# Kernel tuning notes

Measured on AMD Instinct MI355X. Metric: run time of the kernel, lower is better.

## Reference

```python
import jax, jax.numpy as jnp
import numpy as np

NU, NI = 100000, 50000          # sampled users / items in the block
E = 1600000                      # edges (user-item interactions)
D = 64                           # hidden_dims
R = 6                            # num_ratings + 1


def setup_inputs() -> dict:
    key = jax.random.key(0)
    ks = jax.random.split(key, 24)
    f = jax.random.normal
    inp = {
        'user_ids': jax.random.randint(ks[0], (NU,), 0, 500000),
        'item_ids': jax.random.randint(ks[1], (NI,), 0, 200000),
        'gender': jax.random.randint(ks[2], (NU,), 0, 3),
        'genres': jax.random.randint(ks[3], (NI,), 0, 20),
        'edge_user': jax.random.randint(ks[4], (E,), 0, NU),
        'edge_item': jax.random.randint(ks[5], (E,), 0, NI),
        'rating': jax.random.randint(ks[6], (E,), 0, R),
        'user_emb': f(ks[7], (500000, D), jnp.float32),
        'item_emb': f(ks[8], (200000, D), jnp.float32),
        'gender_emb': f(ks[9], (3, D), jnp.float32),
        'genre_emb': f(ks[10], (20, D), jnp.float32),
        'Wr_watched': f(ks[11], (R, D, D), jnp.float32) * 0.1,
        'Wr_watchedby': f(ks[12], (R, D, D), jnp.float32) * 0.1,
        'Ww': f(ks[13], (D, 2 * D), jnp.float32) * 0.1,
        'bw': f(ks[14], (D,), jnp.float32) * 0.1,
        'Wwb': f(ks[15], (D, 2 * D), jnp.float32) * 0.1,
        'bwb': f(ks[16], (D,), jnp.float32) * 0.1,
        'Wf': f(ks[17], (D, D), jnp.float32) * 0.1,
        'bf': f(ks[18], (D,), jnp.float32) * 0.1,
        'Vf': f(ks[19], (D, D), jnp.float32) * 0.1,
        'bv': f(ks[20], (D,), jnp.float32) * 0.1,
    }
    return inp


def _gcmc_conv(Wr, Wlin, blin, h_src, h_dst, src_idx, dst_idx, rating, n_dst):
    # per-node relation transform: [R, N_src, D] (grouped GEMM instead of per-edge [E,D,D])
    X = jnp.einsum('nj,rij->rni', h_src, Wr)
    m = X[rating, src_idx]                              # per-edge message [E, D]
    s = jax.ops.segment_sum(m, dst_idx, num_segments=n_dst)
    cnt = jax.ops.segment_sum(jnp.ones((m.shape[0], 1), m.dtype), dst_idx,
                              num_segments=n_dst)
    h_neigh = s / jnp.maximum(cnt, 1.0)                 # mean; 0 for isolated nodes
    return jax.nn.relu(jnp.concatenate([h_dst, h_neigh], axis=1) @ Wlin.T + blin)


def reference(user_ids, item_ids, gender, genres, edge_user, edge_item, rating,
              user_emb, item_emb, gender_emb, genre_emb,
              Wr_watched, Wr_watchedby, Ww, bw, Wwb, bwb, Wf, bf, Vf, bv):
    hu = user_emb[user_ids] + gender_emb[gender]        # [NU, D]
    hi = item_emb[item_ids] + genre_emb[genres]         # [NI, D]
    # GCMCLayer: 'watched' (user -> item) and 'watchedby' (item -> user)
    hi_new = _gcmc_conv(Wr_watched, Ww, bw, hu, hi, edge_user, edge_item,
                        rating, hi.shape[0])
    hu_new = _gcmc_conv(Wr_watchedby, Wwb, bwb, hi, hu, edge_item, edge_user,
                        rating, hu.shape[0])
    user_out = hu_new @ Wf.T + bf
    item_out = hi_new @ Vf.T + bv
    return user_out, item_out
```

## Files before the change

### kernel.cpp

```cpp
#include <hip/hip_runtime.h>
#include <hip/hip_bf16.h>

#define D 64
#define NRAT 6

typedef float f32x4 __attribute__((ext_vector_type(4)));
typedef short bf16x8 __attribute__((ext_vector_type(8)));

union FragU { uint32_t u[4]; bf16x8 v; };

__device__ __forceinline__ short f2bf(float f) {
    __hip_bfloat16 h = __float2bfloat16(f);
    union { __hip_bfloat16 h; short s; } c; c.h = h; return c.s;
}
__device__ __forceinline__ uint32_t pk2(float a, float b) {
    union { short s[2]; uint32_t u; } c; c.s[0] = f2bf(a); c.s[1] = f2bf(b); return c.u;
}

__global__ void build_setup(const int* __restrict__ uid, const int* __restrict__ iid,
                            const int* __restrict__ gender, const int* __restrict__ genres,
                            const float* __restrict__ user_emb, const float* __restrict__ item_emb,
                            const float* __restrict__ gender_emb, const float* __restrict__ genre_emb,
                            unsigned short* __restrict__ hu, unsigned short* __restrict__ hi,
                            int* __restrict__ zeroRegion,
                            const float* __restrict__ Wr_w, const float* __restrict__ Wr_wb,
                            const float* __restrict__ Ww, const float* __restrict__ Wwb,
                            const float* __restrict__ Vf, const float* __restrict__ Wf,
                            short* __restrict__ pWrW, short* __restrict__ pWrWB,
                            short* __restrict__ pWw, short* __restrict__ pWwb,
                            short* __restrict__ pVf, short* __restrict__ pWf,
                            int NU, int NI) {
    int t = blockIdx.x * blockDim.x + threadIdx.x;
    if (t < 512) zeroRegion[t] = 0;

    int tp = t - 1024;
    if (tp >= 0 && tp < 73728) {
        const float* src; short* dst; int K; int idx;
        if      (tp < 24576) { src = Wr_w;  dst = pWrW;  K = 64;  idx = tp; }
        else if (tp < 49152) { src = Wr_wb; dst = pWrWB; K = 64;  idx = tp - 24576; }
        else if (tp < 57344) { src = Ww;    dst = pWw;   K = 128; idx = tp - 49152; }
        else if (tp < 65536) { src = Wwb;   dst = pWwb;  K = 128; idx = tp - 57344; }
        else if (tp < 69632) { src = Vf;    dst = pVf;   K = 64;  idx = tp - 65536; }
        else                 { src = Wf;    dst = pWf;   K = 64;  idx = tp - 69632; }
        int per  = 64 * K;
        int sub  = idx / per;
        int li   = idx % per;
        int e    = li & 7;
        int lane = (li >> 3) & 63;
        int frag = li >> 9;
        int nkt  = K >> 5;
        int t16  = frag / nkt, tk = frag % nkt;
        int row  = t16 * 16 + (lane & 15);
        int col  = tk * 32 + (lane >> 4) * 8 + e;
        dst[idx] = f2bf(src[((size_t)(sub * 64 + row)) * K + col]);
    }

    int total = (NU + NI) * 16;
    if (t >= total) return;
    int row = t >> 4, c = t & 15;
    uint2 o;
    if (row < NU) {
        int u = uid[row], g = gender[row];
        float4 a = ((const float4*)user_emb)[(size_t)u * 16 + c];
        float4 b = ((const float4*)gender_emb)[(size_t)g * 16 + c];
        o.x = pk2(a.x + b.x, a.y + b.y); o.y = pk2(a.z + b.z, a.w + b.w);
        ((uint2*)hu)[(size_t)row * 16 + c] = o;
    } else {
        int r2 = row - NU;
        int it = iid[r2], ge = genres[r2];
        float4 a = ((const float4*)item_emb)[(size_t)it * 16 + c];
        float4 b = ((const float4*)genre_emb)[(size_t)ge * 16 + c];
        o.x = pk2(a.x + b.x, a.y + b.y); o.y = pk2(a.z + b.z, a.w + b.w);
        ((uint2*)hi)[(size_t)r2 * 16 + c] = o;
    }
}

__global__ __launch_bounds__(256) void hist_both(const int* __restrict__ edge_item,
                                                 const int* __restrict__ edge_user,
                                                 int* __restrict__ cntI, int* __restrict__ cntU,
                                                 int E) {
    __shared__ int hI[256], hU[256];
    hI[threadIdx.x] = 0; hU[threadIdx.x] = 0;
    __syncthreads();
    for (int i = blockIdx.x * blockDim.x + threadIdx.x; i < E; i += gridDim.x * blockDim.x) {
        atomicAdd(&hI[edge_item[i] >> 8], 1);
        atomicAdd(&hU[edge_user[i] >> 9], 1);
    }
    __syncthreads();
    int vi = hI[threadIdx.x], vu = hU[threadIdx.x];
    if (vi) atomicAdd(&cntI[threadIdx.x], vi);
    if (vu) atomicAdd(&cntU[threadIdx.x], vu);
}

__global__ __launch_bounds__(256) void scan_both(const int* __restrict__ cntI,
                                                 const int* __restrict__ cntU,
                                                 int* __restrict__ offI, int* __restrict__ offU,
                                                 int* __restrict__ curI, int* __restrict__ curU,
                                                 int NBI, int NBU, int E) {
    const int* cnt = blockIdx.x ? cntU : cntI;
    int* coarseOff  = blockIdx.x ? offU : offI;
    int* coarseCur  = blockIdx.x ? curU : curI;
    int NB          = blockIdx.x ? NBU : NBI;
    __shared__ int p[256];
    int tid = threadIdx.x;
    int v = (tid < NB) ? cnt[tid] : 0;
    p[tid] = v; __syncthreads();
    for (int dd = 1; dd < 256; dd <<= 1) {
        int a = (tid >= dd) ? p[tid - dd] : 0;
        __syncthreads();
        p[tid] += a;
        __syncthreads();
    }
    int excl = p[tid] - v;
    if (tid < NB) { coarseOff[tid] = excl; coarseCur[tid] = excl; }
    if (tid == 0) coarseOff[NB] = E;
}

__global__ __launch_bounds__(256) void multisplit_A2(
        const int* __restrict__ edge_item, const int* __restrict__ edge_user,
        const int* __restrict__ rating,
        int* __restrict__ curI, int* __restrict__ curU,
        unsigned* __restrict__ staged1, unsigned* __restrict__ staged2,
        int E, int nTiles, int NU, int NI) {
    const bool dirU = blockIdx.x >= nTiles;
    const int* dst = dirU ? edge_user : edge_item;
    const int* src = dirU ? edge_item : edge_user;
    const int shift = dirU ? 9 : 8;
    const int Ns = dirU ? NI : NU;
    int* coarseCur = dirU ? curU : curI;
    unsigned* staged = dirU ? staged2 : staged1;
    const int tile = (dirU ? blockIdx.x - nTiles : blockIdx.x) * 2048;

    __shared__ unsigned srt[2048];
    __shared__ int sft[2048];
    __shared__ int hist[256], pfx[256], shm[256];
    const int tid = threadIdx.x;
    int cnt = E - tile; if (cnt > 2048) cnt = 2048;
    hist[tid] = 0;
    __syncthreads();
    unsigned rec[8]; int bk[8];
    #pragma unroll
    for (int k = 0; k < 8; ++k) {
        int i = tile + k * 256 + tid;
        bk[k] = -1;
        if (i < E) {
            int d = dst[i], s = src[i], r = rating[i];
            bk[k] = d >> shift;
            rec[k] = (unsigned)(s + r * Ns) | ((unsigned)(d & ((1 << shift) - 1)) << 20);
            atomicAdd(&hist[bk[k]], 1);
        }
    }
    __syncthreads();
    pfx[tid] = hist[tid];
    __syncthreads();
    for (int dd = 1; dd < 256; dd <<= 1) {
        int a = (tid >= dd) ? pfx[tid - dd] : 0;
        __syncthreads();
        pfx[tid] += a;
        __syncthreads();
    }
    int h = hist[tid];
    int excl = pfx[tid] - h;
    int gb = 0;
    if (h > 0) gb = atomicAdd(&coarseCur[tid], h);
    shm[tid] = gb - excl;
    __syncthreads();
    hist[tid] = excl;
    __syncthreads();
    #pragma unroll
    for (int k = 0; k < 8; ++k) {
        if (bk[k] >= 0) {
            int p = atomicAdd(&hist[bk[k]], 1);
            srt[p] = rec[k];
            sft[p] = shm[bk[k]];
        }
    }
    __syncthreads();
    for (int i = tid; i < cnt; i += 256)
        staged[sft[i] + i] = srt[i];
}

__global__ __launch_bounds__(256) void multisplit_B2(
        unsigned* __restrict__ staged1, unsigned* __restrict__ staged2,
        const int* __restrict__ coarseOffI, const int* __restrict__ coarseOffU,
        int* __restrict__ offI, int* __restrict__ offU,
        int NBI, int NU, int NI, int E) {
    const bool dirU = (int)blockIdx.x >= NBI;
    unsigned* staged = dirU ? staged2 : staged1;
    const int* coarseOff = dirU ? coarseOffU : coarseOffI;
    int* off = dirU ? offU : offI;
    const int N = dirU ? NU : NI;
    const int shift = dirU ? 9 : 8;
    const int b = dirU ? blockIdx.x - NBI : blockIdx.x;
    const int nb = dirU ? (N + (1 << 9) - 1) >> 9 : NBI;

    __shared__ unsigned rec[16384];
    __shared__ int hist[512], pfx[512];
    const int tid = threadIdx.x;
    const int range = 1 << shift;
    int cbase = coarseOff[b];
    int cnt = coarseOff[b + 1] - cbase;
    if (cnt > 16384) cnt = 16384;
    hist[tid] = 0; hist[tid + 256] = 0;
    __syncthreads();
    for (int i = tid; i < cnt; i += 256) {
        unsigned x = staged[cbase + i];
        rec[i] = x;
        atomicAdd(&hist[x >> 20], 1);
    }
    __syncthreads();
    pfx[tid] = hist[tid]; pfx[tid + 256] = hist[tid + 256];
    __syncthreads();
    for (int dd = 1; dd < 256; dd <<= 1) {
        int a = (tid >= dd) ? pfx[tid - dd] : 0;
        int c = (tid >= dd) ? pfx[tid + 256 - dd] : 0;
        __syncthreads();
        pfx[tid] += a; pfx[tid + 256] += c;
        __syncthreads();
    }
    int tot0 = pfx[255];
    __syncthreads();
    pfx[tid + 256] += tot0;
    __syncthreads();
    int e0 = pfx[tid] - hist[tid];
    int e1 = pfx[tid + 256] - hist[tid + 256];
    __syncthreads();
    hist[tid] = e0; hist[tid + 256] = e1;
    int dbase = b << shift;
    if (dbase + tid < N) off[dbase + tid] = cbase + e0;
    if (range > 256 && dbase + tid + 256 < N) off[dbase + tid + 256] = cbase + e1;
    if (b == nb - 1 && tid == 0) off[N] = E;
    __syncthreads();
    for (int i = tid; i < cnt; i += 256) {
        unsigned x = rec[i];
        int p = atomicAdd(&hist[x >> 20], 1);
        staged[cbase + p] = x;
    }
}

__global__ __launch_bounds__(256) void pretransform2(
        const unsigned short* __restrict__ hu, const unsigned short* __restrict__ hi,
        const short* __restrict__ pWrW, const short* __restrict__ pWrWB,
        unsigned short* __restrict__ y1, unsigned short* __restrict__ y2,
        int NU, int NI, int wavesU) {
    const int lane = threadIdx.x & 63;
    const int m = lane & 15, q = lane >> 4;
    int wave = (blockIdx.x * blockDim.x + threadIdx.x) >> 6;
    const bool dirI = wave >= wavesU;
    const unsigned short* h = dirI ? hi : hu;
    const short* pWr = dirI ? pWrWB : pWrW;
    unsigned short* y = dirI ? y2 : y1;
    const int Ns = dirI ? NI : NU;
    if (dirI) wave -= wavesU;
    const int n0 = wave * 16;
    if (n0 >= Ns) return;
    int nrow = n0 + m; if (nrow > Ns - 1) nrow = Ns - 1;

    bf16x8 bB[2];
    {
        const unsigned short* ph = h + (size_t)nrow * D + q * 8;
        bB[0] = *(const bf16x8*)(ph);
        bB[1] = *(const bf16x8*)(ph + 32);
    }
    const int srcA = ((q & 1) << 5) + m;
    const int srcB = srcA + 16;
    const bool hiq = (q >> 1) != 0;

    #pragma unroll
    for (int r = 0; r < NRAT; ++r) {
        f32x4 acc[4] = {};
        #pragma unroll
        for (int it = 0; it < 4; ++it)
            #pragma unroll
            for (int kt = 0; kt < 2; ++kt) {
                bf16x8 a = *(const bf16x8*)(pWr + (((r * 4 + it) * 2 + kt) << 9) + (lane << 3));
                acc[it] = __builtin_amdgcn_mfma_f32_16x16x32_bf16(a, bB[kt], acc[it], 0, 0, 0);
            }
        uint32_t u0[4], u1[4];
        #pragma unroll
        for (int it = 0; it < 4; ++it) {
            u0[it] = pk2(acc[it][0], acc[it][1]);
            u1[it] = pk2(acc[it][2], acc[it][3]);
        }
        #pragma unroll
        for (int w = 0; w < 2; ++w) {
            uint32_t aa0 = (uint32_t)__shfl((int)u0[2*w],   srcA), bb0 = (uint32_t)__shfl((int)u0[2*w+1], srcA);
            uint32_t aa1 = (uint32_t)__shfl((int)u1[2*w],   srcA), bb1 = (uint32_t)__shfl((int)u1[2*w+1], srcA);
            uint32_t aa2 = (uint32_t)__shfl((int)u0[2*w],   srcB), bb2 = (uint32_t)__shfl((int)u0[2*w+1], srcB);
            uint32_t aa3 = (uint32_t)__shfl((int)u1[2*w],   srcB), bb3 = (uint32_t)__shfl((int)u1[2*w+1], srcB);
            FragU f;
            f.u[0] = hiq ? bb0 : aa0;
            f.u[1] = hiq ? bb1 : aa1;
            f.u[2] = hiq ? bb2 : aa2;
            f.u[3] = hiq ? bb3 : aa3;
            *(bf16x8*)(y + ((size_t)r * Ns + nrow) * D + w * 32 + q * 8) = f.v;
        }
    }
}

__global__ __launch_bounds__(256) void gather_both(
        const int* __restrict__ offI, const int* __restrict__ offU,
        const unsigned* __restrict__ staged1, const unsigned* __restrict__ staged2,
        const unsigned* __restrict__ y1, const unsigned* __restrict__ y2,
        unsigned* __restrict__ hn1, unsigned* __restrict__ hn2,
        int NI, int NU) {
    const int lane = threadIdx.x & 63;
    const int half = lane >> 5;
    const int l5   = lane & 31;
    int g = (blockIdx.x * blockDim.x + threadIdx.x) >> 6;
    const bool dirU = g >= NI;
    int n = dirU ? g - NI : g;
    if (dirU && n >= NU) return;
    const int* off = dirU ? offU : offI;
    const unsigned* packed = dirU ? staged2 : staged1;
    const unsigned* y = dirU ? y2 : y1;
    unsigned* hn = dirU ? hn2 : hn1;

    int b = off[n], e = off[n + 1];
    float a0 = 0.f, a1 = 0.f;

#define YPAIR(mm) y[(((mm) << 5) & 0x1FFFFE0u) | (unsigned)l5]
#define ACC2(dd) { a0 += __uint_as_float((dd) << 16); \
                   a1 += __uint_as_float((dd) & 0xFFFF0000u); }

    for (int base = b; base < e; base += 64) {
        int idx = base + lane; if (idx > e - 1) idx = e - 1;
        unsigned meta = packed[idx];
        int cnt = e - base; if (cnt > 64) cnt = 64;
        int j = 0;
        for (; j + 4 <= cnt; j += 4) {
            unsigned mA = (unsigned)__shfl((int)meta, j + half);
            unsigned mB = (unsigned)__shfl((int)meta, j + 2 + half);
            unsigned dA = YPAIR(mA);
            unsigned dB = YPAIR(mB);
            ACC2(dA); ACC2(dB);
        }
        if (j + 2 <= cnt) {
            unsigned mA = (unsigned)__shfl((int)meta, j + half);
            unsigned dA = YPAIR(mA);
            ACC2(dA);
            j += 2;
        }
        if (j < cnt) {
            unsigned mm = (unsigned)__builtin_amdgcn_readlane((int)meta, j);
            if (half == 0) { unsigned dd = YPAIR(mm); ACC2(dd); }
        }
    }
#undef YPAIR
#undef ACC2

    float o0 = __shfl(a0, lane ^ 32);
    float o1 = __shfl(a1, lane ^ 32);
    float inv = 1.0f / fmaxf((float)(e - b), 1.0f);
    float s0 = (a0 + o0) * inv;
    float s1 = (a1 + o1) * inv;
    if (lane < 32) hn[(size_t)n * 32 + l5] = pk2(s0, s1);
}

__global__ __launch_bounds__(256) void transform_both(
        const unsigned short* __restrict__ hn1, const unsigned short* __restrict__ hn2,
        const unsigned short* __restrict__ hi, const unsigned short* __restrict__ hu,
        const short* __restrict__ pWw, const short* __restrict__ pWwb,
        const float* __restrict__ bw, const float* __restrict__ bwb,
        const short* __restrict__ pVf, const short* __restrict__ pWf,
        const float* __restrict__ bv, const float* __restrict__ bf,
        float* __restrict__ item_out, float* __restrict__ user_out,
        int NI, int NU, int tilesI) {
    const int lane = threadIdx.x & 63;
    const int m = lane & 15, q = lane >> 4;
    int wave = (blockIdx.x * blockDim.x + threadIdx.x) >> 6;
    const bool dirU = wave >= tilesI;
    if (dirU) wave -= tilesI;
    const unsigned short* hn = dirU ? hn2 : hn1;
    const unsigned short* hd = dirU ? hu : hi;
    const short* pWlin = dirU ? pWwb : pWw;
    const float* blin  = dirU ? bwb : bw;
    const short* pW2   = dirU ? pWf : pVf;
    const float* b2    = dirU ? bf : bv;
    float* out = dirU ? user_out : item_out;
    const int N = dirU ? NU : NI;
    const int n0 = wave * 16;
    if (n0 >= N) return;
    int nrow = n0 + m; if (nrow > N - 1) nrow = N - 1;

    bf16x8 bH[2], bHN[2];
    {
        const unsigned short* ph = hd + (size_t)nrow * D + q * 8;
        bH[0] = *(const bf16x8*)(ph);
        bH[1] = *(const bf16x8*)(ph + 32);
        const unsigned short* pn = hn + (size_t)nrow * D + q * 8;
        bHN[0] = *(const bf16x8*)(pn);
        bHN[1] = *(const bf16x8*)(pn + 32);
    }

    f32x4 acc2[4] = {};
    #pragma unroll
    for (int it = 0; it < 4; ++it)
        #pragma unroll
        for (int kt = 0; kt < 4; ++kt) {
            bf16x8 a = *(const bf16x8*)(pWlin + (((it * 4) + kt) << 9) + (lane << 3));
            bf16x8 b = (kt < 2) ? bH[kt] : bHN[kt - 2];
            acc2[it] = __builtin_amdgcn_mfma_f32_16x16x32_bf16(a, b, acc2[it], 0, 0, 0);
        }

    const int srcA = ((q & 1) << 5) + m;
    const int srcB = srcA + 16;
    const bool hiq = (q >> 1) != 0;
    uint32_t u0[4], u1[4];
    float vbl = blin[lane];
    #pragma unroll
    for (int it = 0; it < 4; ++it) {
        float h0 = fmaxf(acc2[it][0] + __shfl(vbl, it * 16 + q * 4 + 0), 0.f);
        float h1 = fmaxf(acc2[it][1] + __shfl(vbl, it * 16 + q * 4 + 1), 0.f);
        float h2 = fmaxf(acc2[it][2] + __shfl(vbl, it * 16 + q * 4 + 2), 0.f);
        float h3 = fmaxf(acc2[it][3] + __shfl(vbl, it * 16 + q * 4 + 3), 0.f);
        u0[it] = pk2(h0, h1);
        u1[it] = pk2(h2, h3);
    }
    bf16x8 bA3[2];
    #pragma unroll
    for (int w = 0; w < 2; ++w) {
        uint32_t aa0 = (uint32_t)__shfl((int)u0[2*w],   srcA), bb0 = (uint32_t)__shfl((int)u0[2*w+1], srcA);
        uint32_t aa1 = (uint32_t)__shfl((int)u1[2*w],   srcA), bb1 = (uint32_t)__shfl((int)u1[2*w+1], srcA);
        uint32_t aa2 = (uint32_t)__shfl((int)u0[2*w],   srcB), bb2 = (uint32_t)__shfl((int)u0[2*w+1], srcB);
        uint32_t aa3 = (uint32_t)__shfl((int)u1[2*w],   srcB), bb3 = (uint32_t)__shfl((int)u1[2*w+1], srcB);
        FragU f;
        f.u[0] = hiq ? bb0 : aa0;
        f.u[1] = hiq ? bb1 : aa1;
        f.u[2] = hiq ? bb2 : aa2;
        f.u[3] = hiq ? bb3 : aa3;
        bA3[w] = f.v;
    }

    f32x4 acc3[4] = {};
    #pragma unroll
    for (int ct = 0; ct < 4; ++ct)
        #pragma unroll
        for (int kt = 0; kt < 2; ++kt) {
            bf16x8 b = *(const bf16x8*)(pW2 + (((ct * 2) + kt) << 9) + (lane << 3));
            acc3[ct] = __builtin_amdgcn_mfma_f32_16x16x32_bf16(bA3[kt], b, acc3[ct], 0, 0, 0);
        }
    #pragma unroll
    for (int ct = 0; ct < 4; ++ct) {
        float bb = b2[ct * 16 + m];
        #pragma unroll
        for (int rg = 0; rg < 4; ++rg) {
            int n = n0 + q * 4 + rg;
            if (n < N) out[(size_t)n * D + ct * 16 + m] = acc3[ct][rg] + bb;
        }
    }
}

extern "C" void kernel_launch(void* const* d_in, const int* in_sizes, int n_in,
                              void* d_out, int out_size, void* d_ws, size_t ws_size,
                              hipStream_t stream) {
    const int*   user_ids   = (const int*)  d_in[0];
    const int*   item_ids   = (const int*)  d_in[1];
    const int*   gender     = (const int*)  d_in[2];
    const int*   genres     = (const int*)  d_in[3];
    const int*   edge_user  = (const int*)  d_in[4];
    const int*   edge_item  = (const int*)  d_in[5];
    const int*   rating     = (const int*)  d_in[6];
    const float* user_emb   = (const float*)d_in[7];
    const float* item_emb   = (const float*)d_in[8];
    const float* gender_emb = (const float*)d_in[9];
    const float* genre_emb  = (const float*)d_in[10];
    const float* Wr_watched   = (const float*)d_in[11];
    const float* Wr_watchedby = (const float*)d_in[12];
    const float* Ww  = (const float*)d_in[13];
    const float* bw  = (const float*)d_in[14];
    const float* Wwb = (const float*)d_in[15];
    const float* bwb = (const float*)d_in[16];
    const float* Wf  = (const float*)d_in[17];
    const float* bf  = (const float*)d_in[18];
    const float* Vf  = (const float*)d_in[19];
    const float* bv  = (const float*)d_in[20];

    const int NU = in_sizes[0];
    const int NI = in_sizes[1];
    const int E  = in_sizes[4];
    const int NBI = (NI + 255) >> 8;
    const int NBU = (NU + 511) >> 9;

    float* out_f    = (float*)d_out;
    float* user_out = out_f;
    float* item_out = out_f + (size_t)NU * D;

    unsigned short* hu  = (unsigned short*)d_ws;
    unsigned short* hi  = hu  + (size_t)NU * D;
    unsigned short* hn1 = hi  + (size_t)NI * D;
    unsigned short* hn2 = hn1 + (size_t)NI * D;
    unsigned short* y1  = hn2 + (size_t)NU * D;
    unsigned short* y2  = y1  + (size_t)NRAT * NU * D;
    size_t bfElems = (size_t)(2 * NU + 2 * NI) * D + (size_t)NRAT * (NU + NI) * D;
    size_t byteOff = (bfElems * 2 + 15) & ~(size_t)15;
    short* pWrW  = (short*)((char*)d_ws + byteOff);
    short* pWrWB = pWrW  + 24576;
    short* pWw   = pWrWB + 24576;
    short* pWwb  = pWw   + 8192;
    short* pVf   = pWwb  + 8192;
    short* pWf   = pVf   + 4096;
    int* coarseCntI = (int*)(pWf + 4096);
    int* coarseCntU = coarseCntI + 256;
    int* coarseOffI = coarseCntU + 256;
    int* coarseOffU = coarseOffI + 257;
    int* coarseCurI = coarseOffU + 257;
    int* coarseCurU = coarseCurI + 256;
    int* offI   = coarseCurU + 256;
    int* offU   = offI + NI + 1;
    unsigned* staged1 = (unsigned*)(offU + NU + 1);
    unsigned* staged2 = staged1 + E;

    int totalh = (NU + NI) * 16;
    build_setup<<<(totalh + 255) / 256, 256, 0, stream>>>(
        user_ids, item_ids, gender, genres,
        user_emb, item_emb, gender_emb, genre_emb, hu, hi, coarseCntI,
        Wr_watched, Wr_watchedby, Ww, Wwb, Vf, Wf,
        pWrW, pWrWB, pWw, pWwb, pVf, pWf, NU, NI);

    hist_both<<<512, 256, 0, stream>>>(edge_item, edge_user, coarseCntI, coarseCntU, E);
    scan_both<<<2, 256, 0, stream>>>(coarseCntI, coarseCntU, coarseOffI, coarseOffU,
                                     coarseCurI, coarseCurU, NBI, NBU, E);

    const int nTilesA = (E + 2047) / 2048;
    multisplit_A2<<<2 * nTilesA, 256, 0, stream>>>(edge_item, edge_user, rating,
                                                   coarseCurI, coarseCurU,
                                                   staged1, staged2, E, nTilesA, NU, NI);
    multisplit_B2<<<NBI + NBU, 256, 0, stream>>>(staged1, staged2, coarseOffI, coarseOffU,
                                                 offI, offU, NBI, NU, NI, E);

    {
        int wavesU = (NU + 15) / 16, wavesI = (NI + 15) / 16;
        int blocks = (wavesU + wavesI + 3) / 4;
        pretransform2<<<blocks, 256, 0, stream>>>(hu, hi, pWrW, pWrWB, y1, y2, NU, NI, wavesU);
    }
    gather_both<<<(NI + NU + 3) / 4, 256, 0, stream>>>(offI, offU, staged1, staged2,
                                                       (const unsigned*)y1, (const unsigned*)y2,
                                                       (unsigned*)hn1, (unsigned*)hn2, NI, NU);
    {
        int tilesI = (NI + 15) / 16, tilesU = (NU + 15) / 16;
        int blocks = (tilesI + tilesU + 3) / 4;
        transform_both<<<blocks, 256, 0, stream>>>(hn1, hn2, hi, hu, pWw, pWwb, bw, bwb,
                                                   pVf, pWf, bv, bf, item_out, user_out,
                                                   NI, NU, tilesI);
    }
}
```

Before: 236.6 us.

## Fuse pretransform into multisplit launch and widen gather to four edges per step

The per-rating pretransform GEMM moves into the multisplit_A launch as extra blocks. This removes one kernel launch and lets the MFMA work overlap the bucketing pass. The gather kernel now has each quarter-wave load 8 bytes per lane (uint2), so four edges are processed per step instead of two. The partial sums are then reduced with xor shuffles. The fused kernel carries the multisplit's shared-memory footprint on the transform blocks, which may reduce their occupancy.

```diff
diff --git a/kernel.cpp b/kernel.cpp
--- a/kernel.cpp
+++ b/kernel.cpp
@@ -116,25 +116,86 @@
     if (tid == 0) coarseOff[NB] = E;
 }
 
-__global__ __launch_bounds__(256) void multisplit_A2(
+__global__ __launch_bounds__(256) void msA_pre(
         const int* __restrict__ edge_item, const int* __restrict__ edge_user,
         const int* __restrict__ rating,
         int* __restrict__ curI, int* __restrict__ curU,
         unsigned* __restrict__ staged1, unsigned* __restrict__ staged2,
-        int E, int nTiles, int NU, int NI) {
-    const bool dirU = blockIdx.x >= nTiles;
+        const unsigned short* __restrict__ hu, const unsigned short* __restrict__ hi,
+        const short* __restrict__ pWrW, const short* __restrict__ pWrWB,
+        unsigned short* __restrict__ y1, unsigned short* __restrict__ y2,
+        int E, int nTiles, int NU, int NI, int wavesU) {
+    __shared__ unsigned srt[2048];
+    __shared__ int sft[2048];
+    __shared__ int hist[256], pfx[256], shm[256];
+    const int tid = threadIdx.x;
+
+    if ((int)blockIdx.x >= 2 * nTiles) {
+        const int lane = tid & 63;
+        const int m = lane & 15, q = lane >> 4;
+        int wave = (((int)blockIdx.x - 2 * nTiles) * 256 + tid) >> 6;
+        const bool dirI = wave >= wavesU;
+        const unsigned short* h = dirI ? hi : hu;
+        const short* pWr = dirI ? pWrWB : pWrW;
+        unsigned short* y = dirI ? y2 : y1;
+        const int Ns = dirI ? NI : NU;
+        if (dirI) wave -= wavesU;
+        const int n0 = wave * 16;
+        if (n0 >= Ns) return;
+        int nrow = n0 + m; if (nrow > Ns - 1) nrow = Ns - 1;
+
+        bf16x8 bB[2];
+        {
+            const unsigned short* ph = h + (size_t)nrow * D + q * 8;
+            bB[0] = *(const bf16x8*)(ph);
+            bB[1] = *(const bf16x8*)(ph + 32);
+        }
+        const int srcA = ((q & 1) << 5) + m;
+        const int srcB = srcA + 16;
+        const bool hiq = (q >> 1) != 0;
+
+        #pragma unroll
+        for (int r = 0; r < NRAT; ++r) {
+            f32x4 acc[4] = {};
+            #pragma unroll
+            for (int it = 0; it < 4; ++it)
+                #pragma unroll
+                for (int kt = 0; kt < 2; ++kt) {
+                    bf16x8 a = *(const bf16x8*)(pWr + (((r * 4 + it) * 2 + kt) << 9) + (lane << 3));
+                    acc[it] = __builtin_amdgcn_mfma_f32_16x16x32_bf16(a, bB[kt], acc[it], 0, 0, 0);
+                }
+            uint32_t u0[4], u1[4];
+            #pragma unroll
+            for (int it = 0; it < 4; ++it) {
+                u0[it] = pk2(acc[it][0], acc[it][1]);
+                u1[it] = pk2(acc[it][2], acc[it][3]);
+            }
+            #pragma unroll
+            for (int w = 0; w < 2; ++w) {
+                uint32_t aa0 = (uint32_t)__shfl((int)u0[2*w],   srcA), bb0 = (uint32_t)__shfl((int)u0[2*w+1], srcA);
+                uint32_t aa1 = (uint32_t)__shfl((int)u1[2*w],   srcA), bb1 = (uint32_t)__shfl((int)u1[2*w+1], srcA);
+                uint32_t aa2 = (uint32_t)__shfl((int)u0[2*w],   srcB), bb2 = (uint32_t)__shfl((int)u0[2*w+1], srcB);
+                uint32_t aa3 = (uint32_t)__shfl((int)u1[2*w],   srcB), bb3 = (uint32_t)__shfl((int)u1[2*w+1], srcB);
+                FragU f;
+                f.u[0] = hiq ? bb0 : aa0;
+                f.u[1] = hiq ? bb1 : aa1;
+                f.u[2] = hiq ? bb2 : aa2;
+                f.u[3] = hiq ? bb3 : aa3;
+                *(bf16x8*)(y + ((size_t)r * Ns + nrow) * D + w * 32 + q * 8) = f.v;
+            }
+        }
+        return;
+    }
+
+    const bool dirU = (int)blockIdx.x >= nTiles;
     const int* dst = dirU ? edge_user : edge_item;
     const int* src = dirU ? edge_item : edge_user;
     const int shift = dirU ? 9 : 8;
     const int Ns = dirU ? NI : NU;
     int* coarseCur = dirU ? curU : curI;
     unsigned* staged = dirU ? staged2 : staged1;
-    const int tile = (dirU ? blockIdx.x - nTiles : blockIdx.x) * 2048;
-
-    __shared__ unsigned srt[2048];
-    __shared__ int sft[2048];
-    __shared__ int hist[256], pfx[256], shm[256];
-    const int tid = threadIdx.x;
+    const int tile = (dirU ? (int)blockIdx.x - nTiles : (int)blockIdx.x) * 2048;
+
     int cnt = E - tile; if (cnt > 2048) cnt = 2048;
     hist[tid] = 0;
     __syncthreads();
@@ -238,90 +299,32 @@
     }
 }
 
-__global__ __launch_bounds__(256) void pretransform2(
-        const unsigned short* __restrict__ hu, const unsigned short* __restrict__ hi,
-        const short* __restrict__ pWrW, const short* __restrict__ pWrWB,
-        unsigned short* __restrict__ y1, unsigned short* __restrict__ y2,
-        int NU, int NI, int wavesU) {
-    const int lane = threadIdx.x & 63;
-    const int m = lane & 15, q = lane >> 4;
-    int wave = (blockIdx.x * blockDim.x + threadIdx.x) >> 6;
-    const bool dirI = wave >= wavesU;
-    const unsigned short* h = dirI ? hi : hu;
-    const short* pWr = dirI ? pWrWB : pWrW;
-    unsigned short* y = dirI ? y2 : y1;
-    const int Ns = dirI ? NI : NU;
-    if (dirI) wave -= wavesU;
-    const int n0 = wave * 16;
-    if (n0 >= Ns) return;
-    int nrow = n0 + m; if (nrow > Ns - 1) nrow = Ns - 1;
-
-    bf16x8 bB[2];
-    {
-        const unsigned short* ph = h + (size_t)nrow * D + q * 8;
-        bB[0] = *(const bf16x8*)(ph);
-        bB[1] = *(const bf16x8*)(ph + 32);
-    }
-    const int srcA = ((q & 1) << 5) + m;
-    const int srcB = srcA + 16;
-    const bool hiq = (q >> 1) != 0;
-
-    #pragma unroll
-    for (int r = 0; r < NRAT; ++r) {
-        f32x4 acc[4] = {};
-        #pragma unroll
-        for (int it = 0; it < 4; ++it)
-            #pragma unroll
-            for (int kt = 0; kt < 2; ++kt) {
-                bf16x8 a = *(const bf16x8*)(pWr + (((r * 4 + it) * 2 + kt) << 9) + (lane << 3));
-                acc[it] = __builtin_amdgcn_mfma_f32_16x16x32_bf16(a, bB[kt], acc[it], 0, 0, 0);
-            }
-        uint32_t u0[4], u1[4];
-        #pragma unroll
-        for (int it = 0; it < 4; ++it) {
-            u0[it] = pk2(acc[it][0], acc[it][1]);
-            u1[it] = pk2(acc[it][2], acc[it][3]);
-        }
-        #pragma unroll
-        for (int w = 0; w < 2; ++w) {
-            uint32_t aa0 = (uint32_t)__shfl((int)u0[2*w],   srcA), bb0 = (uint32_t)__shfl((int)u0[2*w+1], srcA);
-            uint32_t aa1 = (uint32_t)__shfl((int)u1[2*w],   srcA), bb1 = (uint32_t)__shfl((int)u1[2*w+1], srcA);
-            uint32_t aa2 = (uint32_t)__shfl((int)u0[2*w],   srcB), bb2 = (uint32_t)__shfl((int)u0[2*w+1], srcB);
-            uint32_t aa3 = (uint32_t)__shfl((int)u1[2*w],   srcB), bb3 = (uint32_t)__shfl((int)u1[2*w+1], srcB);
-            FragU f;
-            f.u[0] = hiq ? bb0 : aa0;
-            f.u[1] = hiq ? bb1 : aa1;
-            f.u[2] = hiq ? bb2 : aa2;
-            f.u[3] = hiq ? bb3 : aa3;
-            *(bf16x8*)(y + ((size_t)r * Ns + nrow) * D + w * 32 + q * 8) = f.v;
-        }
-    }
-}
-
 __global__ __launch_bounds__(256) void gather_both(
         const int* __restrict__ offI, const int* __restrict__ offU,
         const unsigned* __restrict__ staged1, const unsigned* __restrict__ staged2,
-        const unsigned* __restrict__ y1, const unsigned* __restrict__ y2,
-        unsigned* __restrict__ hn1, unsigned* __restrict__ hn2,
+        const uint2* __restrict__ y1, const uint2* __restrict__ y2,
+        uint2* __restrict__ hn1, uint2* __restrict__ hn2,
         int NI, int NU) {
     const int lane = threadIdx.x & 63;
-    const int half = lane >> 5;
-    const int l5   = lane & 31;
+    const int qt = lane >> 4;
+    const int t  = lane & 15;
     int g = (blockIdx.x * blockDim.x + threadIdx.x) >> 6;
     const bool dirU = g >= NI;
     int n = dirU ? g - NI : g;
     if (dirU && n >= NU) return;
     const int* off = dirU ? offU : offI;
     const unsigned* packed = dirU ? staged2 : staged1;
-    const unsigned* y = dirU ? y2 : y1;
-    unsigned* hn = dirU ? hn2 : hn1;
+    const uint2* y = dirU ? y2 : y1;
+    uint2* hn = dirU ? hn2 : hn1;
 
     int b = off[n], e = off[n + 1];
-    float a0 = 0.f, a1 = 0.f;
-
-#define YPAIR(mm) y[(((mm) << 5) & 0x1FFFFE0u) | (unsigned)l5]
-#define ACC2(dd) { a0 += __uint_as_float((dd) << 16); \
-                   a1 += __uint_as_float((dd) & 0xFFFF0000u); }
+    float a0 = 0.f, a1 = 0.f, a2 = 0.f, a3 = 0.f;
+
+#define YROW(mm) y[(((mm) & 0xFFFFFu) << 4) | (unsigned)t]
+#define ACC4(dd) { a0 += __uint_as_float((dd).x << 16);          \
+                   a1 += __uint_as_float((dd).x & 0xFFFF0000u);  \
+                   a2 += __uint_as_float((dd).y << 16);          \
+                   a3 += __uint_as_float((dd).y & 0xFFFF0000u); }
 
     for (int base = b; base < e; base += 64) {
         int idx = base + lane; if (idx > e - 1) idx = e - 1;
@@ -329,32 +332,32 @@
         int cnt = e - base; if (cnt > 64) cnt = 64;
         int j = 0;
         for (; j + 4 <= cnt; j += 4) {
-            unsigned mA = (unsigned)__shfl((int)meta, j + half);
-            unsigned mB = (unsigned)__shfl((int)meta, j + 2 + half);
-            unsigned dA = YPAIR(mA);
-            unsigned dB = YPAIR(mB);
-            ACC2(dA); ACC2(dB);
-        }
-        if (j + 2 <= cnt) {
-            unsigned mA = (unsigned)__shfl((int)meta, j + half);
-            unsigned dA = YPAIR(mA);
-            ACC2(dA);
-            j += 2;
-        }
-        if (j < cnt) {
-            unsigned mm = (unsigned)__builtin_amdgcn_readlane((int)meta, j);
-            if (half == 0) { unsigned dd = YPAIR(mm); ACC2(dd); }
-        }
-    }
-#undef YPAIR
-#undef ACC2
-
-    float o0 = __shfl(a0, lane ^ 32);
-    float o1 = __shfl(a1, lane ^ 32);
+            unsigned mm = (unsigned)__shfl((int)meta, j + qt);
+            uint2 dd = YROW(mm);
+            ACC4(dd);
+        }
+        int rem = cnt - j;
+        if (rem > 0) {
+            unsigned mm = (unsigned)__shfl((int)meta, j + qt);
+            uint2 dd = YROW(mm);
+            if (qt < rem) { ACC4(dd); }
+        }
+    }
+#undef YROW
+#undef ACC4
+
+    a0 += __shfl_xor(a0, 16); a1 += __shfl_xor(a1, 16);
+    a2 += __shfl_xor(a2, 16); a3 += __shfl_xor(a3, 16);
+    a0 += __shfl_xor(a0, 32); a1 += __shfl_xor(a1, 32);
+    a2 += __shfl_xor(a2, 32); a3 += __shfl_xor(a3, 32);
+
     float inv = 1.0f / fmaxf((float)(e - b), 1.0f);
-    float s0 = (a0 + o0) * inv;
-    float s1 = (a1 + o1) * inv;
-    if (lane < 32) hn[(size_t)n * 32 + l5] = pk2(s0, s1);
+    if (lane < 16) {
+        uint2 o;
+        o.x = pk2(a0 * inv, a1 * inv);
+        o.y = pk2(a2 * inv, a3 * inv);
+        hn[(size_t)n * 16 + t] = o;
+    }
 }
 
 __global__ __launch_bounds__(256) void transform_both(
@@ -523,20 +526,18 @@
                                      coarseCurI, coarseCurU, NBI, NBU, E);
 
     const int nTilesA = (E + 2047) / 2048;
-    multisplit_A2<<<2 * nTilesA, 256, 0, stream>>>(edge_item, edge_user, rating,
-                                                   coarseCurI, coarseCurU,
-                                                   staged1, staged2, E, nTilesA, NU, NI);
+    const int wavesU = (NU + 15) / 16, wavesI = (NI + 15) / 16;
+    const int ptBlocks = (wavesU + wavesI + 3) / 4;
+    msA_pre<<<2 * nTilesA + ptBlocks, 256, 0, stream>>>(
+        edge_item, edge_user, rating, coarseCurI, coarseCurU, staged1, staged2,
+        hu, hi, pWrW, pWrWB, y1, y2, E, nTilesA, NU, NI, wavesU);
+
     multisplit_B2<<<NBI + NBU, 256, 0, stream>>>(staged1, staged2, coarseOffI, coarseOffU,
                                                  offI, offU, NBI, NU, NI, E);
 
-    {
-        int wavesU = (NU + 15) / 16, wavesI = (NI + 15) / 16;
-        int blocks = (wavesU + wavesI + 3) / 4;
-        pretransform2<<<blocks, 256, 0, stream>>>(hu, hi, pWrW, pWrWB, y1, y2, NU, NI, wavesU);
-    }
     gather_both<<<(NI + NU + 3) / 4, 256, 0, stream>>>(offI, offU, staged1, staged2,
-                                                       (const unsigned*)y1, (const unsigned*)y2,
-                                                       (unsigned*)hn1, (unsigned*)hn2, NI, NU);
+                                                       (const uint2*)y1, (const uint2*)y2,
+                                                       (uint2*)hn1, (uint2*)hn2, NI, NU);
     {
         int tilesI = (NI + 15) / 16, tilesU = (NU + 15) / 16;
         int blocks = (tilesI + tilesU + 3) / 4;
```

New measurement: 236.3 us. No clear change (-0.1%).
